# Kernel tuning notes

Hardware: AMD Instinct MI355X
Metric: run time of the kernel (lower is better)

The kernel has to match this reference:

```python
import jax, jax.numpy as jnp
import numpy as np

B, S, E, H = 4, 2048, 1024, 16
D = E // H  # head dim = 64


def setup_inputs() -> dict:
    key = jax.random.key(0)
    ks = jax.random.split(key, 9)
    s_in = 1.0 / np.sqrt(E)
    return {
        "x": jax.random.normal(ks[0], (B, S, E), dtype=jnp.float32),
        # stacked per-head projection weights, acting as x @ W + b
        "Wq": jax.random.normal(ks[1], (H, E, D), dtype=jnp.float32) * s_in,
        "bq": jax.random.normal(ks[2], (H, D), dtype=jnp.float32) * 0.01,
        "Wk": jax.random.normal(ks[3], (H, E, D), dtype=jnp.float32) * s_in,
        "bk": jax.random.normal(ks[4], (H, D), dtype=jnp.float32) * 0.01,
        "Wv": jax.random.normal(ks[5], (H, E, D), dtype=jnp.float32) * s_in,
        "bv": jax.random.normal(ks[6], (H, D), dtype=jnp.float32) * 0.01,
        "Wo": jax.random.normal(ks[7], (E, E), dtype=jnp.float32) * s_in,
        "bo": jax.random.normal(ks[8], (E,), dtype=jnp.float32) * 0.01,
    }


def reference(x, Wq, bq, Wk, bk, Wv, bv, Wo, bo):
    # Batched per-head projections (equivalent to the per-head nn.Linear loop)
    q = jnp.einsum("bse,hed->bhsd", x, Wq) + bq[None, :, None, :]
    k = jnp.einsum("bse,hed->bhsd", x, Wk) + bk[None, :, None, :]
    v = jnp.einsum("bse,hed->bhsd", x, Wv) + bv[None, :, None, :]
    scale = 1.0 / jnp.sqrt(jnp.asarray(D, dtype=x.dtype))
    scores = jnp.einsum("bhsd,bhtd->bhst", q, k) * scale  # [B,H,S,S]
    attn = jax.nn.softmax(scores, axis=-1)
    ctx = jnp.einsum("bhst,bhtd->bhsd", attn, v)  # [B,H,S,D]
    # torch.cat over heads along last dim -> [B,S,H*D]=[B,S,E]
    ctx = jnp.transpose(ctx, (0, 2, 1, 3)).reshape(x.shape[0], x.shape[1], E)
    return ctx @ Wo + bo
```

## Files before the change

### kernel.cpp

```cpp
#include <hip/hip_runtime.h>
#include <math.h>

#define B_ 4
#define S_ 2048
#define E_ 1024
#define H_ 16
#define D_ 64
#define BH_ (B_ * H_)

#define SCALE_LOG2E 0.18033688011112042f

typedef short short8 __attribute__((ext_vector_type(8)));
typedef float f32x4 __attribute__((ext_vector_type(4)));

static __device__ __forceinline__ unsigned short f2bf(float f) {
    unsigned int u = __float_as_uint(f);
    unsigned int r = (u + 0x7fffu + ((u >> 16) & 1u)) >> 16;
    return (unsigned short)r;
}

static __device__ __forceinline__ unsigned int pack_bf16_trunc(float hi, float lo) {
    return __builtin_amdgcn_perm(__float_as_uint(hi), __float_as_uint(lo), 0x07060302u);
}

static __device__ __forceinline__ void gl_lds16(const unsigned short* g, unsigned short* l) {
    __builtin_amdgcn_global_load_lds(
        (const __attribute__((address_space(1))) unsigned int*)g,
        (__attribute__((address_space(3))) unsigned int*)l, 16, 0, 0);
}


__global__ __launch_bounds__(256) void xcvt_kernel(
    const float* __restrict__ x, unsigned short* __restrict__ Xb)
{
    size_t i = ((size_t)blockIdx.x * 256 + threadIdx.x) * 8;
    float4 a = *(const float4*)&x[i];
    float4 b = *(const float4*)&x[i + 4];
    ushort4 u0, u1;
    u0.x = f2bf(a.x); u0.y = f2bf(a.y); u0.z = f2bf(a.z); u0.w = f2bf(a.w);
    u1.x = f2bf(b.x); u1.y = f2bf(b.y); u1.z = f2bf(b.z); u1.w = f2bf(b.w);
    *(ushort4*)&Xb[i]     = u0;
    *(ushort4*)&Xb[i + 4] = u1;
}

__global__ __launch_bounds__(256) void wtrans_qkv_kernel(
    const float* __restrict__ Wq, const float* __restrict__ Wk,
    const float* __restrict__ Wv, unsigned short* __restrict__ Wt)
{
    __shared__ float t[32][33];
    const int tx = threadIdx.x & 31, ty = threadIdx.x >> 5;
    const int r0 = blockIdx.x * 32, c0 = blockIdx.y * 32;
    const int z = blockIdx.z, mtx = z >> 4, h = z & 15;
    const float* s = (mtx == 0 ? Wq : (mtx == 1 ? Wk : Wv)) + (size_t)h * E_ * D_;
    const float scale = (mtx == 0) ? SCALE_LOG2E : 1.0f;
    unsigned short* d = Wt + (size_t)mtx * E_ * E_ + (size_t)h * D_ * E_;
#pragma unroll
    for (int i = 0; i < 4; ++i)
        t[ty + i * 8][tx] = s[(size_t)(r0 + ty + i * 8) * D_ + c0 + tx];
    __syncthreads();
#pragma unroll
    for (int i = 0; i < 4; ++i)
        d[(size_t)(c0 + ty + i * 8) * E_ + r0 + tx] = f2bf(t[tx][ty + i * 8] * scale);
}

__global__ __launch_bounds__(256) void wtrans_kernel(
    const float* __restrict__ src, unsigned short* __restrict__ dst, int R, int C)
{
    __shared__ float t[32][33];
    const int tx = threadIdx.x & 31, ty = threadIdx.x >> 5;
    const int r0 = blockIdx.x * 32, c0 = blockIdx.y * 32;
#pragma unroll
    for (int i = 0; i < 4; ++i)
        t[ty + i * 8][tx] = src[(size_t)(r0 + ty + i * 8) * C + c0 + tx];
    __syncthreads();
#pragma unroll
    for (int i = 0; i < 4; ++i)
        dst[(size_t)(c0 + ty + i * 8) * R + r0 + tx] = f2bf(t[tx][ty + i * 8]);
}

__global__ __launch_bounds__(256) void qkv_gemm_kernel(
    const unsigned short* __restrict__ Xb, const unsigned short* __restrict__ Wt,
    const float* __restrict__ bq, const float* __restrict__ bk,
    const float* __restrict__ bv,
    unsigned short* __restrict__ Qh, unsigned short* __restrict__ Kh,
    unsigned short* __restrict__ Vth)
{
    __shared__ unsigned short As[2][128 * 64];
    __shared__ unsigned short Bs[2][128 * 64];
    const int tid = threadIdx.x;
    const int lane = tid & 63, wid = tid >> 6;
    const int quad = lane >> 4, lc = lane & 15;
    const int wm = wid >> 1, wn = wid & 1;
    const int m0 = blockIdx.y * 128, n0 = blockIdx.x * 128;
    const int l8 = lane >> 3;
    const int sch = ((lane & 7) ^ l8) * 8;

    f32x4 acc[4][4];
#pragma unroll
    for (int mt = 0; mt < 4; ++mt)
#pragma unroll
        for (int nt = 0; nt < 4; ++nt)
            acc[mt][nt] = (f32x4){0.f, 0.f, 0.f, 0.f};

#pragma unroll
    for (int i = 0; i < 4; ++i) {
        int rw = wid * 32 + i * 8;
        gl_lds16(&Xb[(size_t)(m0 + rw + l8) * E_ + sch], &As[0][rw * 64]);
        gl_lds16(&Wt[(size_t)(n0 + rw + l8) * E_ + sch], &Bs[0][rw * 64]);
    }
    __syncthreads();

    for (int k0 = 0; k0 < E_; k0 += 64) {
        const int cur = (k0 >> 6) & 1;
        if (k0 + 64 < E_) {
#pragma unroll
            for (int i = 0; i < 4; ++i) {
                int rw = wid * 32 + i * 8;
                gl_lds16(&Xb[(size_t)(m0 + rw + l8) * E_ + k0 + 64 + sch], &As[cur ^ 1][rw * 64]);
                gl_lds16(&Wt[(size_t)(n0 + rw + l8) * E_ + k0 + 64 + sch], &Bs[cur ^ 1][rw * 64]);
            }
        }
#pragma unroll
        for (int kc = 0; kc < 2; ++kc) {
            short8 a[4], bfr[4];
#pragma unroll
            for (int mt = 0; mt < 4; ++mt)
                a[mt] = *(const short8*)&As[cur][(wm * 64 + mt * 16 + lc) * 64 +
                                                (((kc * 4 + quad) ^ (lc & 7)) << 3)];
#pragma unroll
            for (int nt = 0; nt < 4; ++nt)
                bfr[nt] = *(const short8*)&Bs[cur][(wn * 64 + nt * 16 + lc) * 64 +
                                                  (((kc * 4 + quad) ^ (lc & 7)) << 3)];
#pragma unroll
            for (int mt = 0; mt < 4; ++mt)
#pragma unroll
                for (int nt = 0; nt < 4; ++nt)
                    acc[mt][nt] = __builtin_amdgcn_mfma_f32_16x16x32_bf16(
                        a[mt], bfr[nt], acc[mt][nt], 0, 0, 0);
        }
        __syncthreads();
    }

    const int nb = n0 + wn * 64;
    const int mtx = nb >> 10;
    const int h = (nb >> 6) & 15;
    const int sg0 = m0 + wm * 64;
    const int bb_ = sg0 >> 11;
    if (mtx < 2) {
        const float bsc = (mtx == 0) ? SCALE_LOG2E : 1.0f;
        const float* bias = (mtx == 0 ? bq : bk) + h * D_;
        unsigned short* Out = (mtx == 0) ? Qh : Kh;
#pragma unroll
        for (int nt = 0; nt < 4; ++nt) {
            int d = nt * 16 + lc;
            float bb = bias[d] * bsc;
#pragma unroll
            for (int mt = 0; mt < 4; ++mt)
#pragma unroll
                for (int r = 0; r < 4; ++r) {
                    int ss = (sg0 + mt * 16 + quad * 4 + r) & (S_ - 1);
                    Out[((size_t)(bb_ * H_ + h) * S_ + ss) * D_ + d] =
                        f2bf(acc[mt][nt][r] + bb);
                }
        }
    } else {
        const float* bias = bv + h * D_;
#pragma unroll
        for (int nt = 0; nt < 4; ++nt) {
            int d = nt * 16 + lc;
            float bb = bias[d];
#pragma unroll
            for (int mt = 0; mt < 4; ++mt) {
                int ss0 = (sg0 + mt * 16 + quad * 4) & (S_ - 1);
                ushort4 u;
                u.x = f2bf(acc[mt][nt][0] + bb);
                u.y = f2bf(acc[mt][nt][1] + bb);
                u.z = f2bf(acc[mt][nt][2] + bb);
                u.w = f2bf(acc[mt][nt][3] + bb);
                *(ushort4*)&Vth[(((size_t)bb_ * H_ + h) * D_ + d) * S_ + ss0] = u;
            }
        }
    }
}

__global__ __launch_bounds__(256) void attn_kernel(
    const unsigned short* __restrict__ Qh, const unsigned short* __restrict__ Kh,
    const unsigned short* __restrict__ Vth, unsigned short* __restrict__ Ch)
{
    __shared__ unsigned short ps[256 * 64];
    __shared__ unsigned short ks[2][64 * 64];
    __shared__ unsigned short vt[2][64 * 64];
    const int tid = threadIdx.x;
    const int lane = tid & 63, wid = tid >> 6;
    const int quad = lane >> 4, lc = lane & 15;
    const int bh = blockIdx.x, b = bh >> 4, h = bh & 15;
    const int q0 = blockIdx.y * 256;
    const size_t base  = (size_t)bh * S_ * D_;
    const size_t vbase = (size_t)bh * D_ * S_;
    const int l8 = lane >> 3;
    const int sch = ((lane & 7) ^ l8) * 8;

#pragma unroll
    for (int i = 0; i < 8; ++i) {
        int rw = wid * 64 + i * 8;
        gl_lds16(&Qh[base + (size_t)(q0 + rw + l8) * D_ + sch], &ps[rw * 64]);
    }
#pragma unroll
    for (int i = 0; i < 2; ++i) {
        int rw = wid * 16 + i * 8;
        gl_lds16(&Kh[base + (size_t)(rw + l8) * D_ + sch], &ks[0][rw * 64]);
        gl_lds16(&Vth[vbase + (size_t)(rw + l8) * S_ + sch], &vt[0][rw * 64]);
    }
    __syncthreads();
    short8 qf[4][2];
#pragma unroll
    for (int mt = 0; mt < 4; ++mt)
#pragma unroll
        for (int kc = 0; kc < 2; ++kc)
            qf[mt][kc] = *(const short8*)&ps[(wid * 64 + mt * 16 + lc) * 64 +
                                             (((kc * 4 + quad) ^ (lc & 7)) << 3)];

    short8 ones;
#pragma unroll
    for (int i = 0; i < 8; ++i) ones[i] = (short)0x3F80;

    f32x4 ctx[4][4], lacc[4];
#pragma unroll
    for (int mt = 0; mt < 4; ++mt) {
        lacc[mt] = (f32x4){0.f, 0.f, 0.f, 0.f};
#pragma unroll
        for (int nt = 0; nt < 4; ++nt)
            ctx[mt][nt] = (f32x4){0.f, 0.f, 0.f, 0.f};
    }

    for (int kt = 0; kt < S_; kt += 64) {
        const int cur = (kt >> 6) & 1;
        if (kt + 64 < S_) {
#pragma unroll
            for (int i = 0; i < 2; ++i) {
                int rw = wid * 16 + i * 8;
                gl_lds16(&Kh[base + (size_t)(kt + 64 + rw + l8) * D_ + sch],
                         &ks[cur ^ 1][rw * 64]);
                gl_lds16(&Vth[vbase + (size_t)(rw + l8) * S_ + kt + 64 + sch],
                         &vt[cur ^ 1][rw * 64]);
            }
        }

        f32x4 st[4][4];
#pragma unroll
        for (int mtK = 0; mtK < 4; ++mtK)
#pragma unroll
            for (int ntQ = 0; ntQ < 4; ++ntQ)
                st[mtK][ntQ] = (f32x4){0.f, 0.f, 0.f, 0.f};
#pragma unroll
        for (int kc = 0; kc < 2; ++kc) {
            short8 kf[4];
#pragma unroll
            for (int mtK = 0; mtK < 4; ++mtK)
                kf[mtK] = *(const short8*)&ks[cur][(mtK * 16 + lc) * 64 +
                                                  (((kc * 4 + quad) ^ (lc & 7)) << 3)];
#pragma unroll
            for (int mtK = 0; mtK < 4; ++mtK)
#pragma unroll
                for (int ntQ = 0; ntQ < 4; ++ntQ)
                    st[mtK][ntQ] = __builtin_amdgcn_mfma_f32_16x16x32_bf16(
                        kf[mtK], qf[ntQ][kc], st[mtK][ntQ], 0, 0, 0);
        }

#pragma unroll
        for (int ntQ = 0; ntQ < 4; ++ntQ) {
            const int prow = (wid * 64 + ntQ * 16 + lc) * 64 + ((quad & 1) << 2);
#pragma unroll
            for (int mtK = 0; mtK < 4; ++mtK) {
                float p0 = __builtin_amdgcn_exp2f(st[mtK][ntQ][0]);
                float p1 = __builtin_amdgcn_exp2f(st[mtK][ntQ][1]);
                float p2 = __builtin_amdgcn_exp2f(st[mtK][ntQ][2]);
                float p3 = __builtin_amdgcn_exp2f(st[mtK][ntQ][3]);
                uint2 pk;
                pk.x = pack_bf16_trunc(p1, p0);
                pk.y = pack_bf16_trunc(p3, p2);
                *(uint2*)&ps[prow + (((mtK * 2 + (quad >> 1)) ^ (lc & 7)) << 3)] = pk;
            }
        }

#pragma unroll
        for (int kc = 0; kc < 2; ++kc) {
            short8 pf[4], vf[4];
#pragma unroll
            for (int mt = 0; mt < 4; ++mt)
                pf[mt] = *(const short8*)&ps[(wid * 64 + mt * 16 + lc) * 64 +
                                             (((kc * 4 + quad) ^ (lc & 7)) << 3)];
#pragma unroll
            for (int nt = 0; nt < 4; ++nt)
                vf[nt] = *(const short8*)&vt[cur][(nt * 16 + lc) * 64 +
                                                 (((kc * 4 + quad) ^ (lc & 7)) << 3)];
#pragma unroll
            for (int mt = 0; mt < 4; ++mt) {
#pragma unroll
                for (int nt = 0; nt < 4; ++nt)
                    ctx[mt][nt] = __builtin_amdgcn_mfma_f32_16x16x32_bf16(
                        pf[mt], vf[nt], ctx[mt][nt], 0, 0, 0);
                lacc[mt] = __builtin_amdgcn_mfma_f32_16x16x32_bf16(
                    pf[mt], ones, lacc[mt], 0, 0, 0);
            }
        }
        __syncthreads();
    }

#pragma unroll
    for (int mt = 0; mt < 4; ++mt) {
#pragma unroll
        for (int r = 0; r < 4; ++r) {
            float inv = 1.f / lacc[mt][r];
            int row = q0 + wid * 64 + mt * 16 + quad * 4 + r;
#pragma unroll
            for (int nt = 0; nt < 4; ++nt)
                Ch[((size_t)b * S_ + row) * E_ + h * D_ + nt * 16 + lc] =
                    f2bf(ctx[mt][nt][r] * inv);
        }
    }
}

__global__ __launch_bounds__(256) void out_proj_kernel(
    const unsigned short* __restrict__ Ch, const unsigned short* __restrict__ Wot,
    const float* __restrict__ bo, float* __restrict__ out)
{
    __shared__ unsigned short As[2][128 * 64];
    __shared__ unsigned short Bs[2][128 * 64];
    const int tid = threadIdx.x;
    const int lane = tid & 63, wid = tid >> 6;
    const int quad = lane >> 4, lc = lane & 15;
    const int wm = wid >> 1, wn = wid & 1;
    const int m0 = blockIdx.y * 128, n0 = blockIdx.x * 128;
    const int l8 = lane >> 3;
    const int sch = ((lane & 7) ^ l8) * 8;

    f32x4 acc[4][4];
#pragma unroll
    for (int mt = 0; mt < 4; ++mt)
#pragma unroll
        for (int nt = 0; nt < 4; ++nt)
            acc[mt][nt] = (f32x4){0.f, 0.f, 0.f, 0.f};

#pragma unroll
    for (int i = 0; i < 4; ++i) {
        int rw = wid * 32 + i * 8;
        gl_lds16(&Ch[(size_t)(m0 + rw + l8) * E_ + sch], &As[0][rw * 64]);
        gl_lds16(&Wot[(size_t)(n0 + rw + l8) * E_ + sch], &Bs[0][rw * 64]);
    }
    __syncthreads();

    for (int k0 = 0; k0 < E_; k0 += 64) {
        const int cur = (k0 >> 6) & 1;
        if (k0 + 64 < E_) {
#pragma unroll
            for (int i = 0; i < 4; ++i) {
                int rw = wid * 32 + i * 8;
                gl_lds16(&Ch[(size_t)(m0 + rw + l8) * E_ + k0 + 64 + sch], &As[cur ^ 1][rw * 64]);
                gl_lds16(&Wot[(size_t)(n0 + rw + l8) * E_ + k0 + 64 + sch], &Bs[cur ^ 1][rw * 64]);
            }
        }
#pragma unroll
        for (int kc = 0; kc < 2; ++kc) {
            short8 a[4], bfr[4];
#pragma unroll
            for (int mt = 0; mt < 4; ++mt)
                a[mt] = *(const short8*)&As[cur][(wm * 64 + mt * 16 + lc) * 64 +
                                                (((kc * 4 + quad) ^ (lc & 7)) << 3)];
#pragma unroll
            for (int nt = 0; nt < 4; ++nt)
                bfr[nt] = *(const short8*)&Bs[cur][(wn * 64 + nt * 16 + lc) * 64 +
                                                  (((kc * 4 + quad) ^ (lc & 7)) << 3)];
#pragma unroll
            for (int mt = 0; mt < 4; ++mt)
#pragma unroll
                for (int nt = 0; nt < 4; ++nt)
                    acc[mt][nt] = __builtin_amdgcn_mfma_f32_16x16x32_bf16(
                        a[mt], bfr[nt], acc[mt][nt], 0, 0, 0);
        }
        __syncthreads();
    }

#pragma unroll
    for (int mt = 0; mt < 4; ++mt)
#pragma unroll
        for (int nt = 0; nt < 4; ++nt) {
            int n = n0 + wn * 64 + nt * 16 + lc;
            float bb = bo[n];
#pragma unroll
            for (int r = 0; r < 4; ++r) {
                int row = m0 + wm * 64 + mt * 16 + quad * 4 + r;
                out[(size_t)row * E_ + n] = acc[mt][nt][r] + bb;
            }
        }
}

extern "C" void kernel_launch(void* const* d_in, const int* in_sizes, int n_in,
                              void* d_out, int out_size, void* d_ws, size_t ws_size,
                              hipStream_t stream)
{
    const float* x  = (const float*)d_in[0];
    const float* Wq = (const float*)d_in[1];
    const float* bq = (const float*)d_in[2];
    const float* Wk = (const float*)d_in[3];
    const float* bk = (const float*)d_in[4];
    const float* Wv = (const float*)d_in[5];
    const float* bv = (const float*)d_in[6];
    const float* Wo = (const float*)d_in[7];
    const float* bo = (const float*)d_in[8];
    (void)in_sizes; (void)n_in; (void)out_size; (void)ws_size;

    const size_t N = (size_t)BH_ * S_ * D_;
    unsigned short* Wt  = (unsigned short*)d_ws;
    unsigned short* Wot = Wt + (size_t)3072 * 1024;
    unsigned short* Xb  = Wot + (size_t)1024 * 1024;
    unsigned short* Qh  = Xb + N;
    unsigned short* Kh  = Qh + N;
    unsigned short* Vth = Kh + N;
    unsigned short* Ch  = Vth + N;

    xcvt_kernel<<<dim3(4096), 256, 0, stream>>>(x, Xb);
    wtrans_qkv_kernel<<<dim3(32, 2, 48), 256, 0, stream>>>(Wq, Wk, Wv, Wt);
    wtrans_kernel<<<dim3(32, 32, 1), 256, 0, stream>>>(Wo, Wot, E_, E_);

    qkv_gemm_kernel<<<dim3(24, 64), 256, 0, stream>>>(Xb, Wt, bq, bk, bv, Qh, Kh, Vth);
    attn_kernel<<<dim3(64, 8), 256, 0, stream>>>(Qh, Kh, Vth, Ch);
    out_proj_kernel<<<dim3(8, 64), 256, 0, stream>>>(Ch, Wot, bo, (float*)d_out);
}
```

Baseline: 277.6 us.

## Keep attention probabilities in registers via 32x32 MFMA and permlane swap

Rewrites the attention inner loop around 32x32x16 bf16 MFMAs. The score-tile layout is arranged so exp'd probabilities can be repacked into A-operands in registers with v_permlane32_swap, which removes the P round-trip through LDS and the large ps buffer. Each block now handles 128 queries instead of 256 and the grid doubles, so launch_bounds asks for 4 blocks per CU. The aim is less LDS traffic and higher occupancy, at the cost of relying on the exact MFMA output-lane layout, which is tricky to get right.

```diff
diff --git a/kernel.cpp b/kernel.cpp
--- a/kernel.cpp
+++ b/kernel.cpp
@@ -12,6 +12,7 @@
 
 typedef short short8 __attribute__((ext_vector_type(8)));
 typedef float f32x4 __attribute__((ext_vector_type(4)));
+typedef float f32x16 __attribute__((ext_vector_type(16)));
 
 static __device__ __forceinline__ unsigned short f2bf(float f) {
     unsigned int u = __float_as_uint(f);
@@ -183,28 +184,39 @@
     }
 }
 
-__global__ __launch_bounds__(256) void attn_kernel(
+__global__ __launch_bounds__(256, 4) void attn_kernel(
     const unsigned short* __restrict__ Qh, const unsigned short* __restrict__ Kh,
     const unsigned short* __restrict__ Vth, unsigned short* __restrict__ Ch)
 {
-    __shared__ unsigned short ps[256 * 64];
     __shared__ unsigned short ks[2][64 * 64];
     __shared__ unsigned short vt[2][64 * 64];
     const int tid = threadIdx.x;
     const int lane = tid & 63, wid = tid >> 6;
-    const int quad = lane >> 4, lc = lane & 15;
+    const int l31 = lane & 31, hi = lane >> 5;
     const int bh = blockIdx.x, b = bh >> 4, h = bh & 15;
-    const int q0 = blockIdx.y * 256;
+    const int q0 = blockIdx.y * 128;
     const size_t base  = (size_t)bh * S_ * D_;
     const size_t vbase = (size_t)bh * D_ * S_;
     const int l8 = lane >> 3;
     const int sch = ((lane & 7) ^ l8) * 8;
 
-#pragma unroll
-    for (int i = 0; i < 8; ++i) {
-        int rw = wid * 64 + i * 8;
-        gl_lds16(&Qh[base + (size_t)(q0 + rw + l8) * D_ + sch], &ps[rw * 64]);
-    }
+    unsigned short* qstage = &ks[0][0];
+#pragma unroll
+    for (int i = 0; i < 4; ++i) {
+        int rw = wid * 32 + i * 8;
+        gl_lds16(&Qh[base + (size_t)(q0 + rw + l8) * D_ + sch], &qstage[rw * 64]);
+    }
+    __syncthreads();
+    short8 qf[4];
+    {
+        const int qrow = wid * 32 + l31;
+#pragma unroll
+        for (int kc = 0; kc < 4; ++kc)
+            qf[kc] = *(const short8*)&qstage[qrow * 64 +
+                                             (((kc * 2 + hi) ^ (qrow & 7)) << 3)];
+    }
+    __syncthreads();
+
 #pragma unroll
     for (int i = 0; i < 2; ++i) {
         int rw = wid * 16 + i * 8;
@@ -212,26 +224,14 @@
         gl_lds16(&Vth[vbase + (size_t)(rw + l8) * S_ + sch], &vt[0][rw * 64]);
     }
     __syncthreads();
-    short8 qf[4][2];
-#pragma unroll
-    for (int mt = 0; mt < 4; ++mt)
-#pragma unroll
-        for (int kc = 0; kc < 2; ++kc)
-            qf[mt][kc] = *(const short8*)&ps[(wid * 64 + mt * 16 + lc) * 64 +
-                                             (((kc * 4 + quad) ^ (lc & 7)) << 3)];
 
     short8 ones;
 #pragma unroll
     for (int i = 0; i < 8; ++i) ones[i] = (short)0x3F80;
 
-    f32x4 ctx[4][4], lacc[4];
-#pragma unroll
-    for (int mt = 0; mt < 4; ++mt) {
-        lacc[mt] = (f32x4){0.f, 0.f, 0.f, 0.f};
-#pragma unroll
-        for (int nt = 0; nt < 4; ++nt)
-            ctx[mt][nt] = (f32x4){0.f, 0.f, 0.f, 0.f};
-    }
+    f32x16 ctx[2], lacc;
+#pragma unroll
+    for (int i = 0; i < 16; ++i) { ctx[0][i] = 0.f; ctx[1][i] = 0.f; lacc[i] = 0.f; }
 
     for (int kt = 0; kt < S_; kt += 64) {
         const int cur = (kt >> 6) & 1;
@@ -246,78 +246,60 @@
             }
         }
 
-        f32x4 st[4][4];
-#pragma unroll
-        for (int mtK = 0; mtK < 4; ++mtK)
-#pragma unroll
-            for (int ntQ = 0; ntQ < 4; ++ntQ)
-                st[mtK][ntQ] = (f32x4){0.f, 0.f, 0.f, 0.f};
-#pragma unroll
-        for (int kc = 0; kc < 2; ++kc) {
-            short8 kf[4];
-#pragma unroll
-            for (int mtK = 0; mtK < 4; ++mtK)
-                kf[mtK] = *(const short8*)&ks[cur][(mtK * 16 + lc) * 64 +
-                                                  (((kc * 4 + quad) ^ (lc & 7)) << 3)];
-#pragma unroll
-            for (int mtK = 0; mtK < 4; ++mtK)
-#pragma unroll
-                for (int ntQ = 0; ntQ < 4; ++ntQ)
-                    st[mtK][ntQ] = __builtin_amdgcn_mfma_f32_16x16x32_bf16(
-                        kf[mtK], qf[ntQ][kc], st[mtK][ntQ], 0, 0, 0);
-        }
-
-#pragma unroll
-        for (int ntQ = 0; ntQ < 4; ++ntQ) {
-            const int prow = (wid * 64 + ntQ * 16 + lc) * 64 + ((quad & 1) << 2);
-#pragma unroll
-            for (int mtK = 0; mtK < 4; ++mtK) {
-                float p0 = __builtin_amdgcn_exp2f(st[mtK][ntQ][0]);
-                float p1 = __builtin_amdgcn_exp2f(st[mtK][ntQ][1]);
-                float p2 = __builtin_amdgcn_exp2f(st[mtK][ntQ][2]);
-                float p3 = __builtin_amdgcn_exp2f(st[mtK][ntQ][3]);
-                uint2 pk;
-                pk.x = pack_bf16_trunc(p1, p0);
-                pk.y = pack_bf16_trunc(p3, p2);
-                *(uint2*)&ps[prow + (((mtK * 2 + (quad >> 1)) ^ (lc & 7)) << 3)] = pk;
-            }
-        }
-
-#pragma unroll
-        for (int kc = 0; kc < 2; ++kc) {
-            short8 pf[4], vf[4];
-#pragma unroll
-            for (int mt = 0; mt < 4; ++mt)
-                pf[mt] = *(const short8*)&ps[(wid * 64 + mt * 16 + lc) * 64 +
-                                             (((kc * 4 + quad) ^ (lc & 7)) << 3)];
-#pragma unroll
-            for (int nt = 0; nt < 4; ++nt)
-                vf[nt] = *(const short8*)&vt[cur][(nt * 16 + lc) * 64 +
-                                                 (((kc * 4 + quad) ^ (lc & 7)) << 3)];
-#pragma unroll
-            for (int mt = 0; mt < 4; ++mt) {
-#pragma unroll
-                for (int nt = 0; nt < 4; ++nt)
-                    ctx[mt][nt] = __builtin_amdgcn_mfma_f32_16x16x32_bf16(
-                        pf[mt], vf[nt], ctx[mt][nt], 0, 0, 0);
-                lacc[mt] = __builtin_amdgcn_mfma_f32_16x16x32_bf16(
-                    pf[mt], ones, lacc[mt], 0, 0, 0);
+#pragma unroll
+        for (int kb = 0; kb < 2; ++kb) {
+            f32x16 st;
+#pragma unroll
+            for (int i = 0; i < 16; ++i) st[i] = 0.f;
+            const int krow = kb * 32 + l31;
+#pragma unroll
+            for (int kc = 0; kc < 4; ++kc) {
+                short8 kf = *(const short8*)&ks[cur][krow * 64 +
+                                                    (((kc * 2 + hi) ^ (krow & 7)) << 3)];
+                st = __builtin_amdgcn_mfma_f32_32x32x16_bf16(kf, qf[kc], st, 0, 0, 0);
+            }
+
+#pragma unroll
+            for (int ks16 = 0; ks16 < 2; ++ks16) {
+                float e0 = __builtin_amdgcn_exp2f(st[8 * ks16 + 0]);
+                float e1 = __builtin_amdgcn_exp2f(st[8 * ks16 + 1]);
+                float e2 = __builtin_amdgcn_exp2f(st[8 * ks16 + 2]);
+                float e3 = __builtin_amdgcn_exp2f(st[8 * ks16 + 3]);
+                float e4 = __builtin_amdgcn_exp2f(st[8 * ks16 + 4]);
+                float e5 = __builtin_amdgcn_exp2f(st[8 * ks16 + 5]);
+                float e6 = __builtin_amdgcn_exp2f(st[8 * ks16 + 6]);
+                float e7 = __builtin_amdgcn_exp2f(st[8 * ks16 + 7]);
+                unsigned int w0 = pack_bf16_trunc(e1, e0);
+                unsigned int w1 = pack_bf16_trunc(e3, e2);
+                unsigned int w2 = pack_bf16_trunc(e5, e4);
+                unsigned int w3 = pack_bf16_trunc(e7, e6);
+                asm("v_permlane32_swap_b32 %0, %1" : "+v"(w0), "+v"(w2));
+                asm("v_permlane32_swap_b32 %0, %1" : "+v"(w1), "+v"(w3));
+                union { unsigned int u[4]; short8 s; } pu;
+                pu.u[0] = w0; pu.u[1] = w1; pu.u[2] = w2; pu.u[3] = w3;
+                const short8 pf = pu.s;
+
+                lacc = __builtin_amdgcn_mfma_f32_32x32x16_bf16(pf, ones, lacc, 0, 0, 0);
+#pragma unroll
+                for (int dsub = 0; dsub < 2; ++dsub) {
+                    const int vrow = dsub * 32 + l31;
+                    short8 vf = *(const short8*)&vt[cur][vrow * 64 +
+                        (((kb * 4 + ks16 * 2 + hi) ^ (vrow & 7)) << 3)];
+                    ctx[dsub] = __builtin_amdgcn_mfma_f32_32x32x16_bf16(
+                        pf, vf, ctx[dsub], 0, 0, 0);
+                }
             }
         }
         __syncthreads();
     }
 
 #pragma unroll
-    for (int mt = 0; mt < 4; ++mt) {
-#pragma unroll
-        for (int r = 0; r < 4; ++r) {
-            float inv = 1.f / lacc[mt][r];
-            int row = q0 + wid * 64 + mt * 16 + quad * 4 + r;
-#pragma unroll
-            for (int nt = 0; nt < 4; ++nt)
-                Ch[((size_t)b * S_ + row) * E_ + h * D_ + nt * 16 + lc] =
-                    f2bf(ctx[mt][nt][r] * inv);
-        }
+    for (int r = 0; r < 16; ++r) {
+        float inv = 1.f / lacc[r];
+        int q = q0 + wid * 32 + (r & 3) + ((r >> 2) << 3) + hi * 4;
+        size_t rowbase = ((size_t)b * S_ + q) * E_ + h * D_;
+        Ch[rowbase + l31]      = f2bf(ctx[0][r] * inv);
+        Ch[rowbase + 32 + l31] = f2bf(ctx[1][r] * inv);
     }
 }
 
@@ -424,6 +406,6 @@
     wtrans_kernel<<<dim3(32, 32, 1), 256, 0, stream>>>(Wo, Wot, E_, E_);
 
     qkv_gemm_kernel<<<dim3(24, 64), 256, 0, stream>>>(Xb, Wt, bq, bk, bv, Qh, Kh, Vth);
-    attn_kernel<<<dim3(64, 8), 256, 0, stream>>>(Qh, Kh, Vth, Ch);
+    attn_kernel<<<dim3(64, 16), 256, 0, stream>>>(Qh, Kh, Vth, Ch);
     out_proj_kernel<<<dim3(8, 64), 256, 0, stream>>>(Ch, Wot, bo, (float*)d_out);
 }
```

Measured after the change: 275.2 us. Within noise of the previous version (-0.9%).
